# Kernel tuning notes

Hardware: AMD Instinct MI355X
Metric: run time of the kernel (lower is better)

Reference implementation:

```python
import jax, jax.numpy as jnp
import numpy as np

B, N, IN_F = 16, 1024, 256
HEADS, OUT_F = 4, 64
NEG_SLOPE = 0.2
CLAMP_MIN = -1e9
MASK_VAL = -9e15


def setup_inputs() -> dict:
    key = jax.random.key(0)
    k1, k2, k3, k4 = jax.random.split(key, 4)
    x = jax.random.normal(k1, (B, N, IN_F), dtype=jnp.float32)
    adj = jax.random.randint(k2, (B, N, N), 0, 2, dtype=jnp.int32)
    # Linear weight, stored as (in, heads*out) so y = x @ W (xavier-uniform scale)
    lim_w = float(np.sqrt(6.0 / (IN_F + HEADS * OUT_F)))
    W = jax.random.uniform(k3, (IN_F, HEADS * OUT_F), dtype=jnp.float32,
                           minval=-lim_w, maxval=lim_w)
    lim_a = float(np.sqrt(6.0 / (2 * OUT_F + HEADS)))
    a = jax.random.uniform(k4, (2 * OUT_F, HEADS), dtype=jnp.float32,
                           minval=-lim_a, maxval=lim_a)
    return {"x": x, "adj": adj, "W": W, "a": a}


def reference(x, adj, W, a):
    Bs, Ns, _ = x.shape
    # Projection: (B,N,H,D)
    h = (x @ W).reshape(Bs, Ns, HEADS, OUT_F)
    # cat([h_i, h_j]) . a == h_i . a_src + h_j . a_dst  (exact same math, no O(N^2*2D) tensor)
    a_src, a_dst = a[:OUT_F], a[OUT_F:]          # each (D, H)
    s_src = jnp.einsum('bnhd,dh->bnh', h, a_src)  # score contribution of node i
    s_dst = jnp.einsum('bnhd,dh->bnh', h, a_dst)  # score contribution of node j
    e = jax.nn.leaky_relu(s_src[:, :, None, :] + s_dst[:, None, :, :],
                          negative_slope=NEG_SLOPE)  # (B,N,N,H)
    # match original: subtract unmasked row max, clamp, then mask, then softmax over j
    e = e - jnp.max(e, axis=2, keepdims=True)
    e = jnp.maximum(e, CLAMP_MIN)
    att = jnp.where(adj[..., None] > 0, e, MASK_VAL)
    att = jax.nn.softmax(att, axis=2)
    h_prime = jnp.einsum('bijh,bjhd->bihd', att, h)  # (B,N,H,D)
    return h_prime.reshape(Bs, Ns, HEADS * OUT_F)
```

## Files before the change

kernel.cpp:

```cpp
#include <hip/hip_runtime.h>
#include <hip/hip_bf16.h>

#define B_   16
#define N_   1024
#define INF_ 256
#define NH_  4
#define HD_  256
#define L2E  1.4426950408889634f

typedef __attribute__((ext_vector_type(8))) short short8;
typedef __attribute__((ext_vector_type(4))) float f32x4;

__device__ __forceinline__ float bf2f(unsigned short u) {
    union { unsigned int i; float f; } v; v.i = ((unsigned int)u) << 16; return v.f;
}
__device__ __forceinline__ unsigned short f2bf(float f) {
    union { float f; unsigned int i; } v; v.f = f;
    unsigned int x = v.i;
    return (unsigned short)((x + 0x7fffu + ((x >> 16) & 1u)) >> 16);
}
__device__ __forceinline__ unsigned int cvt_pk_bf16(float lo, float hi) {
    unsigned int r;
    asm("v_cvt_pk_bf16_f32 %0, %1, %2" : "=v"(r) : "v"(lo), "v"(hi));
    return r;
}

__global__ __launch_bounds__(256) void k_prep(const int* __restrict__ adj,
                                              const float* __restrict__ W,
                                              unsigned int* __restrict__ pb,
                                              unsigned short* __restrict__ wswz)
{
    int bx = blockIdx.x, t = threadIdx.x;
    if (bx < 2048) {
        int wave = t >> 6, lane = t & 63;
        int row = bx * 8 + wave * 2 + (lane >> 5);
        int w   = lane & 31;
        const int4* ar = (const int4*)(adj + ((long)row << 10) + w * 32);
        unsigned int u = 0;
        #pragma unroll
        for (int k = 0; k < 8; k++) {
            int4 a = ar[k];
            u |= ((unsigned)a.x) << (4 * k);
            u |= ((unsigned)a.y) << (4 * k + 1);
            u |= ((unsigned)a.z) << (4 * k + 2);
            u |= ((unsigned)a.w) << (4 * k + 3);
        }
        pb[((long)w << 14) + row] = u;
    } else {
        int slot = (bx - 2048) * 256 + t;
        int kstep = slot >> 10;
        int nt    = (slot >> 6) & 15;
        int lane  = slot & 63;
        int k0 = kstep * 32 + (lane >> 4) * 8;
        int n  = nt * 16 + (lane & 15);
        ushort4 o0, o1;
        o0.x = f2bf(W[(k0 + 0) * HD_ + n]);
        o0.y = f2bf(W[(k0 + 1) * HD_ + n]);
        o0.z = f2bf(W[(k0 + 2) * HD_ + n]);
        o0.w = f2bf(W[(k0 + 3) * HD_ + n]);
        o1.x = f2bf(W[(k0 + 4) * HD_ + n]);
        o1.y = f2bf(W[(k0 + 5) * HD_ + n]);
        o1.z = f2bf(W[(k0 + 6) * HD_ + n]);
        o1.w = f2bf(W[(k0 + 7) * HD_ + n]);
        *(ushort4*)&wswz[(long)slot * 8]     = o0;
        *(ushort4*)&wswz[(long)slot * 8 + 4] = o1;
    }
}

__global__ __launch_bounds__(256, 4) void k_gemm_h(
    const float* __restrict__ x, const float* __restrict__ a,
    const unsigned short* __restrict__ wswz,
    unsigned short* __restrict__ hswz,
    float* __restrict__ esr, float2* __restrict__ edst)
{
    __shared__ unsigned short xls[64][264];
    int t = threadIdx.x;
    int blk = blockIdx.x;
    int row0 = blk * 64;
    int b  = blk >> 4;
    int n0 = row0 & 1023;

    {
        int sr0 = t >> 4, sc = (t & 15) * 16;
        #pragma unroll
        for (int rr = 0; rr < 4; rr++) {
            int sr = sr0 + rr * 16;
            const float* xp = x + (long)(row0 + sr) * INF_ + sc;
            float4 v0 = ((const float4*)xp)[0];
            float4 v1 = ((const float4*)xp)[1];
            float4 v2 = ((const float4*)xp)[2];
            float4 v3 = ((const float4*)xp)[3];
            ushort4 u0 = {f2bf(v0.x), f2bf(v0.y), f2bf(v0.z), f2bf(v0.w)};
            ushort4 u1 = {f2bf(v1.x), f2bf(v1.y), f2bf(v1.z), f2bf(v1.w)};
            ushort4 u2 = {f2bf(v2.x), f2bf(v2.y), f2bf(v2.z), f2bf(v2.w)};
            ushort4 u3 = {f2bf(v3.x), f2bf(v3.y), f2bf(v3.z), f2bf(v3.w)};
            *(ushort4*)&xls[sr][sc]      = u0;
            *(ushort4*)&xls[sr][sc + 4]  = u1;
            *(ushort4*)&xls[sr][sc + 8]  = u2;
            *(ushort4*)&xls[sr][sc + 12] = u3;
        }
    }
    __syncthreads();

    int wave = t >> 6, lane = t & 63, quad = lane >> 4, l15 = lane & 15;
    f32x4 acc[4][4];
    #pragma unroll
    for (int rg = 0; rg < 4; rg++)
        #pragma unroll
        for (int nt = 0; nt < 4; nt++) acc[rg][nt] = (f32x4){0.f, 0.f, 0.f, 0.f};

    #pragma unroll
    for (int ks = 0; ks < 8; ks++) {
        short8 bfr[4];
        #pragma unroll
        for (int nt = 0; nt < 4; nt++)
            bfr[nt] = *(const short8*)(wswz +
                ((long)((ks * 16 + wave * 4 + nt) * 64 + lane)) * 8);
        #pragma unroll
        for (int rg = 0; rg < 4; rg++) {
            short8 af = *(const short8*)&xls[rg * 16 + l15][ks * 32 + quad * 8];
            #pragma unroll
            for (int nt = 0; nt < 4; nt++)
                acc[rg][nt] = __builtin_amdgcn_mfma_f32_16x16x32_bf16(
                    af, bfr[nt], acc[rg][nt], 0, 0, 0);
        }
    }

    int q0 = (quad & 1) * 4;
    #pragma unroll
    for (int rg = 0; rg < 4; rg++) {
        int row0g = row0 + rg * 16;
        int qd = ((row0g & 31) + quad * 4) >> 3;
        long bj32 = row0g >> 5;
        #pragma unroll
        for (int nt = 0; nt < 4; nt++) {
            int dg = wave * 4 + nt;
            long idx8 = (bj32 * 16 + dg) * 64 + qd * 16 + l15;
            ushort4 o = {f2bf(acc[rg][nt][0]), f2bf(acc[rg][nt][1]),
                         f2bf(acc[rg][nt][2]), f2bf(acc[rg][nt][3])};
            *(ushort4*)&hswz[idx8 * 8 + q0] = o;
        }
    }

    float as_[4], ad_[4];
    #pragma unroll
    for (int nt = 0; nt < 4; nt++) {
        int d = nt * 16 + l15;
        as_[nt] = a[d * NH_ + wave];
        ad_[nt] = a[(64 + d) * NH_ + wave];
    }
    #pragma unroll
    for (int rg = 0; rg < 4; rg++) {
        #pragma unroll
        for (int r = 0; r < 4; r++) {
            float ps = acc[rg][0][r] * as_[0] + acc[rg][1][r] * as_[1]
                     + acc[rg][2][r] * as_[2] + acc[rg][3][r] * as_[3];
            float pd = acc[rg][0][r] * ad_[0] + acc[rg][1][r] * ad_[1]
                     + acc[rg][2][r] * ad_[2] + acc[rg][3][r] * ad_[3];
            #pragma unroll
            for (int m = 1; m < 16; m <<= 1) {
                ps += __shfl_xor(ps, m);
                pd += __shfl_xor(pd, m);
            }
            if (l15 == 0) {
                int row = n0 + rg * 16 + quad * 4 + r;
                float s1 = ps * L2E, s2 = pd * L2E;
                esr[((long)b * NH_ + wave) * N_ + row] = __builtin_exp2f(-0.8f * s1);
                edst[((long)b * NH_ + wave) * N_ + row] =
                    make_float2(__builtin_exp2f(s2), __builtin_exp2f(0.2f * s2));
            }
        }
    }
}

__global__ __launch_bounds__(512, 4) void k_attn(
    const unsigned int* __restrict__ pb, const unsigned short* __restrict__ hswz,
    const float* __restrict__ esr, const float2* __restrict__ edst,
    float* __restrict__ out)
{
    __shared__ float2 esb[1024];
    __shared__ uint2 mtab[16];

    int t = threadIdx.x;
    int bid = blockIdx.x;
    int swz = (bid & 7) * 64 + (bid >> 3);
    int b  = swz >> 5;
    int hh = (swz >> 3) & 3;
    int rg = swz & 7;
    int row0 = rg * 128;

    int wave = t >> 6, lane = t & 63, quad = lane >> 4, l15 = lane & 15;

    esb[t]       = edst[((long)(b * NH_ + hh)) * N_ + t];
    esb[t + 512] = edst[((long)(b * NH_ + hh)) * N_ + t + 512];
    if (t < 16) {
        int k = t;
        unsigned int w0 = ((k & 1) ? 0xffffu : 0u) | ((k & 2) ? 0xffff0000u : 0u);
        unsigned int w1 = ((k & 4) ? 0xffffu : 0u) | ((k & 8) ? 0xffff0000u : 0u);
        mtab[k] = make_uint2(w0, w1);
    }
    __syncthreads();

    int irow = row0 + wave * 16 + l15;
    float r0 = esr[((long)(b * NH_ + hh)) * N_ + irow];
    const unsigned int* pbw = pb + ((long)b << 10) + irow;

    f32x4 acc[4], dn;
    #pragma unroll
    for (int i = 0; i < 4; i++) acc[i] = (f32x4){0.f, 0.f, 0.f, 0.f};
    dn = (f32x4){0.f, 0.f, 0.f, 0.f};
    short8 ones;
    #pragma unroll
    for (int i = 0; i < 8; i++) ones[i] = (short)0x3F80;

    int shq = quad * 8;

    #pragma unroll 4
    for (int jc = 0; jc < 32; jc++) {
        unsigned int m0 = (pbw[((long)jc << 14)] >> shq) & 0xffu;
        const f32x4* ej = (const f32x4*)&esb[jc * 32 + quad * 8];

        union { unsigned int u[4]; short8 s; } p0;
        #pragma unroll
        for (int qp = 0; qp < 4; qp++) {
            f32x4 d = ej[qp];
            p0.u[qp] = cvt_pk_bf16(fmaxf(d[0], r0 * d[1]), fmaxf(d[2], r0 * d[3]));
        }
        uint2 ma = mtab[m0 & 15u], mb = mtab[m0 >> 4];
        p0.u[0] &= ma.x; p0.u[1] &= ma.y; p0.u[2] &= mb.x; p0.u[3] &= mb.y;

        long s8 = ((long)(b * 32 + jc)) * 1024;
        #pragma unroll
        for (int idt = 0; idt < 4; idt++) {
            short8 bf = *(const short8*)(hswz + (s8 + (hh * 4 + idt) * 64 + lane) * 8);
            acc[idt] = __builtin_amdgcn_mfma_f32_16x16x32_bf16(p0.s, bf, acc[idt], 0, 0, 0);
        }
        dn = __builtin_amdgcn_mfma_f32_16x16x32_bf16(p0.s, ones, dn, 0, 0, 0);
    }

    float inv[4];
    #pragma unroll
    for (int r = 0; r < 4; r++) inv[r] = 1.0f / dn[r];
    #pragma unroll
    for (int idt = 0; idt < 4; idt++) {
        int col = hh * 64 + idt * 16 + l15;
        #pragma unroll
        for (int r = 0; r < 4; r++) {
            long row_g = (long)b * N_ + row0 + wave * 16 + quad * 4 + r;
            out[row_g * HD_ + col] = acc[idt][r] * inv[r];
        }
    }
}

extern "C" void kernel_launch(void* const* d_in, const int* in_sizes, int n_in,
                              void* d_out, int out_size, void* d_ws, size_t ws_size,
                              hipStream_t stream) {
    const float* x   = (const float*)d_in[0];
    const int*   adj = (const int*)d_in[1];
    const float* W   = (const float*)d_in[2];
    const float* a   = (const float*)d_in[3];
    float* out = (float*)d_out;

    unsigned int* pb      = (unsigned int*)d_ws;
    unsigned short* hswz  = (unsigned short*)(pb + 524288);
    unsigned short* wswz  = hswz + (long)B_ * N_ * HD_;
    float* esr   = (float*)(wswz + INF_ * HD_);
    float2* edst = (float2*)(esr + (long)B_ * NH_ * N_);

    k_prep<<<2080, 256, 0, stream>>>(adj, W, pb, wswz);
    k_gemm_h<<<256, 256, 0, stream>>>(x, a, wswz, hswz, esr, edst);
    k_attn<<<512, 512, 0, stream>>>(pb, hswz, esr, edst, out);
}
```

Before: 150.5 us.

## Split attention K-loop across wave pairs with two row tiles per wave

Each wave now computes two 16-row tiles, so every loaded h B-fragment feeds two MFMAs instead of one. To keep all 8 waves busy, the j dimension is split in half across wave pairs, and partial accumulators and denominators are reduced through shared memory before normalisation. The aim is to halve global/L2 traffic for the h operand per MFMA. The cost is more accumulator registers, an extra LDS buffer of about 40KB that may lower occupancy, and an additional barrier-based reduction step.

Measured after the change: 147.7 us. No clear change (-1.9%).

```diff
diff --git a/kernel.cpp b/kernel.cpp
--- a/kernel.cpp
+++ b/kernel.cpp
@@ -180,6 +180,7 @@
 {
     __shared__ float2 esb[1024];
     __shared__ uint2 mtab[16];
+    __shared__ float accb[4][2][64][20];
 
     int t = threadIdx.x;
     int bid = blockIdx.x;
@@ -190,6 +191,7 @@
     int row0 = rg * 128;
 
     int wave = t >> 6, lane = t & 63, quad = lane >> 4, l15 = lane & 15;
+    int sp = wave & 3, jh = wave >> 2;
 
     esb[t]       = edst[((long)(b * NH_ + hh)) * N_ + t];
     esb[t + 512] = edst[((long)(b * NH_ + hh)) * N_ + t + 512];
@@ -201,14 +203,19 @@
     }
     __syncthreads();
 
-    int irow = row0 + wave * 16 + l15;
-    float r0 = esr[((long)(b * NH_ + hh)) * N_ + irow];
-    const unsigned int* pbw = pb + ((long)b << 10) + irow;
-
-    f32x4 acc[4], dn;
-    #pragma unroll
-    for (int i = 0; i < 4; i++) acc[i] = (f32x4){0.f, 0.f, 0.f, 0.f};
-    dn = (f32x4){0.f, 0.f, 0.f, 0.f};
+    int ir0 = row0 + sp * 32 + l15;
+    float r0 = esr[((long)(b * NH_ + hh)) * N_ + ir0];
+    float r1 = esr[((long)(b * NH_ + hh)) * N_ + ir0 + 16];
+    const unsigned int* pbw = pb + ((long)b << 10) + ir0;
+
+    f32x4 acc0[4], acc1[4], dn0, dn1;
+    #pragma unroll
+    for (int i = 0; i < 4; i++) {
+        acc0[i] = (f32x4){0.f, 0.f, 0.f, 0.f};
+        acc1[i] = (f32x4){0.f, 0.f, 0.f, 0.f};
+    }
+    dn0 = (f32x4){0.f, 0.f, 0.f, 0.f};
+    dn1 = (f32x4){0.f, 0.f, 0.f, 0.f};
     short8 ones;
     #pragma unroll
     for (int i = 0; i < 8; i++) ones[i] = (short)0x3F80;
@@ -216,38 +223,66 @@
     int shq = quad * 8;
 
     #pragma unroll 4
-    for (int jc = 0; jc < 32; jc++) {
-        unsigned int m0 = (pbw[((long)jc << 14)] >> shq) & 0xffu;
-        const f32x4* ej = (const f32x4*)&esb[jc * 32 + quad * 8];
-
-        union { unsigned int u[4]; short8 s; } p0;
+    for (int jc = 0; jc < 16; jc++) {
+        int w = jh * 16 + jc;
+        unsigned int m0 = (pbw[((long)w << 14)] >> shq) & 0xffu;
+        unsigned int m1 = (pbw[((long)w << 14) + 16] >> shq) & 0xffu;
+        const f32x4* ej = (const f32x4*)&esb[w * 32 + quad * 8];
+
+        union { unsigned int u[4]; short8 s; } p0, p1;
         #pragma unroll
         for (int qp = 0; qp < 4; qp++) {
             f32x4 d = ej[qp];
             p0.u[qp] = cvt_pk_bf16(fmaxf(d[0], r0 * d[1]), fmaxf(d[2], r0 * d[3]));
-        }
-        uint2 ma = mtab[m0 & 15u], mb = mtab[m0 >> 4];
-        p0.u[0] &= ma.x; p0.u[1] &= ma.y; p0.u[2] &= mb.x; p0.u[3] &= mb.y;
-
-        long s8 = ((long)(b * 32 + jc)) * 1024;
+            p1.u[qp] = cvt_pk_bf16(fmaxf(d[0], r1 * d[1]), fmaxf(d[2], r1 * d[3]));
+        }
+        uint2 ma0 = mtab[m0 & 15u], mb0 = mtab[m0 >> 4];
+        uint2 ma1 = mtab[m1 & 15u], mb1 = mtab[m1 >> 4];
+        p0.u[0] &= ma0.x; p0.u[1] &= ma0.y; p0.u[2] &= mb0.x; p0.u[3] &= mb0.y;
+        p1.u[0] &= ma1.x; p1.u[1] &= ma1.y; p1.u[2] &= mb1.x; p1.u[3] &= mb1.y;
+
+        long s8 = ((long)(b * 32 + w)) * 1024;
         #pragma unroll
         for (int idt = 0; idt < 4; idt++) {
             short8 bf = *(const short8*)(hswz + (s8 + (hh * 4 + idt) * 64 + lane) * 8);
-            acc[idt] = __builtin_amdgcn_mfma_f32_16x16x32_bf16(p0.s, bf, acc[idt], 0, 0, 0);
-        }
-        dn = __builtin_amdgcn_mfma_f32_16x16x32_bf16(p0.s, ones, dn, 0, 0, 0);
-    }
-
-    float inv[4];
-    #pragma unroll
-    for (int r = 0; r < 4; r++) inv[r] = 1.0f / dn[r];
-    #pragma unroll
-    for (int idt = 0; idt < 4; idt++) {
-        int col = hh * 64 + idt * 16 + l15;
+            acc0[idt] = __builtin_amdgcn_mfma_f32_16x16x32_bf16(p0.s, bf, acc0[idt], 0, 0, 0);
+            acc1[idt] = __builtin_amdgcn_mfma_f32_16x16x32_bf16(p1.s, bf, acc1[idt], 0, 0, 0);
+        }
+        dn0 = __builtin_amdgcn_mfma_f32_16x16x32_bf16(p0.s, ones, dn0, 0, 0, 0);
+        dn1 = __builtin_amdgcn_mfma_f32_16x16x32_bf16(p1.s, ones, dn1, 0, 0, 0);
+    }
+
+    if (jh == 1) {
+        #pragma unroll
+        for (int idt = 0; idt < 4; idt++) {
+            *(f32x4*)&accb[sp][0][lane][idt * 4] = acc0[idt];
+            *(f32x4*)&accb[sp][1][lane][idt * 4] = acc1[idt];
+        }
+        *(f32x4*)&accb[sp][0][lane][16] = dn0;
+        *(f32x4*)&accb[sp][1][lane][16] = dn1;
+    }
+    __syncthreads();
+
+    if (jh == 0) {
+        f32x4 od0 = *(const f32x4*)&accb[sp][0][lane][16];
+        f32x4 od1 = *(const f32x4*)&accb[sp][1][lane][16];
+        float inv0[4], inv1[4];
         #pragma unroll
         for (int r = 0; r < 4; r++) {
-            long row_g = (long)b * N_ + row0 + wave * 16 + quad * 4 + r;
-            out[row_g * HD_ + col] = acc[idt][r] * inv[r];
+            inv0[r] = 1.0f / (dn0[r] + od0[r]);
+            inv1[r] = 1.0f / (dn1[r] + od1[r]);
+        }
+        #pragma unroll
+        for (int idt = 0; idt < 4; idt++) {
+            f32x4 o0 = *(const f32x4*)&accb[sp][0][lane][idt * 4];
+            f32x4 o1 = *(const f32x4*)&accb[sp][1][lane][idt * 4];
+            int col = hh * 64 + idt * 16 + l15;
+            #pragma unroll
+            for (int r = 0; r < 4; r++) {
+                long row_g = (long)b * N_ + row0 + sp * 32 + quad * 4 + r;
+                out[row_g * HD_ + col] = (acc0[idt][r] + o0[r]) * inv0[r];
+                out[(row_g + 16) * HD_ + col] = (acc1[idt][r] + o1[r]) * inv1[r];
+            }
         }
     }
 }
```
